# Kernel optimization log

Measured on AMD Instinct MI355X. Metric: run time of the kernel, lower is better.

Reference implementation:

```python
import jax, jax.numpy as jnp
import numpy as np
from jax import lax

B, C, H = 64, 3, 224
F = 8  # number of 3x3 filters
POOL = (H - 2) // 2  # 111
FEAT = POOL * POOL * F  # 98568


def setup_inputs() -> dict:
    key = jax.random.key(0)
    ks = jax.random.split(key, 8)
    return {
        "x": jax.random.normal(ks[0], (B, C, H, H), dtype=jnp.float32),
        "filters": jax.random.normal(ks[1], (F, 3, 3), dtype=jnp.float32),
        "W1": jax.random.normal(ks[2], (FEAT, 512), dtype=jnp.float32) * 0.01,
        "b1": jax.random.normal(ks[3], (512,), dtype=jnp.float32) * 0.01,
        "W2": jax.random.normal(ks[4], (512, 256), dtype=jnp.float32) * 0.02,
        "b2": jax.random.normal(ks[5], (256,), dtype=jnp.float32) * 0.02,
        "Wo": jax.random.normal(ks[6], (256, 1000), dtype=jnp.float32) * 0.02,
        "bo": jax.random.normal(ks[7], (1000,), dtype=jnp.float32) * 0.02,
    }


def reference(x, filters, W1, b1, W2, b2, Wo, bo):
    # conv_r + conv_g + conv_b == conv(r+g+b, filt) by linearity -> sum channels once
    s = x.sum(axis=1, keepdims=True)  # [B,1,H,H]
    k = filters[:, None, :, :]  # [F,1,3,3] (OIHW)
    conv = lax.conv_general_dilated(
        s, k, window_strides=(1, 1), padding="VALID",
        dimension_numbers=("NCHW", "OIHW", "NCHW"))  # [B,F,222,222]
    conv = jax.nn.relu(conv)
    pooled = lax.reduce_window(
        conv, -jnp.inf, lax.max,
        window_dimensions=(1, 1, 2, 2), window_strides=(1, 1, 2, 2),
        padding="VALID")  # [B,F,111,111]
    flat = pooled.reshape(x.shape[0], -1)  # filter-major layout matches torch cat order
    h = jax.nn.relu(flat @ W1 + b1)
    h = jax.nn.relu(h @ W2 + b2)
    return jax.nn.softmax(h @ Wo + bo, axis=1)
```

## Files before the change

### kernel.cpp

```cpp
#include <hip/hip_runtime.h>
#include <math.h>

#define Bsz 64
#define Himg 224
#define HS (Himg*Himg)
#define PW 111
#define PP (PW*PW)
#define Fn 8
#define FEAT (Fn*PP)
#define FEATP 98592
#define KC 32
#define NT32_TOT 3081
#define NCH 192
#define N1 512
#define N2 256
#define N3 1000
#define RG 8

typedef short short8 __attribute__((ext_vector_type(8)));
typedef float f32x4 __attribute__((ext_vector_type(4)));

#define GLOAD_LDS16(g, l)                                                     \
  __builtin_amdgcn_global_load_lds(                                           \
      (const __attribute__((address_space(1))) void*)(g),                     \
      (__attribute__((address_space(3))) void*)(l), 16, 0, 0)

__device__ __forceinline__ void cvt_hilo(const float* v, short8& hi, short8& lo) {
#pragma unroll
  for (int j = 0; j < 8; j++) {
    unsigned u = __builtin_bit_cast(unsigned, v[j]);
    hi[j] = (short)(u >> 16);
    float hf = __builtin_bit_cast(float, u & 0xFFFF0000u);
    float r = v[j] - hf;
    lo[j] = (short)(__builtin_bit_cast(unsigned, r) >> 16);
  }
}

__device__ __forceinline__ unsigned packhl(float f) {
  unsigned u = __builtin_bit_cast(unsigned, f);
  unsigned hi = u >> 16;
  float hf = __builtin_bit_cast(float, u & 0xFFFF0000u);
  float r = f - hf;
  unsigned lo = __builtin_bit_cast(unsigned, r) >> 16;
  return (hi << 16) | (lo & 0xFFFFu);
}

__device__ __forceinline__ uint4 pack4(float4 f) {
  uint4 o;
  o.x = packhl(f.x); o.y = packhl(f.y); o.z = packhl(f.z); o.w = packhl(f.w);
  return o;
}

__global__ void k_convpool(const float* __restrict__ x, const float* __restrict__ filt,
                           float* __restrict__ flat) {
  int i = blockIdx.x * 256 + threadIdx.x;
  if (i < Bsz * (FEATP - FEAT))
    flat[(size_t)(i / 24) * FEATP + FEAT + (i % 24)] = 0.f;
  if (i >= Bsz * PP) return;
  int b = i / PP, r = i - b * PP;
  int py = r / PW, px = r - py * PW;
  const float* xb = x + (size_t)b * 3 * HS + (size_t)(2 * py) * Himg + 2 * px;
  float p[4][4];
#pragma unroll
  for (int dy = 0; dy < 4; dy++) {
    const float* row = xb + dy * Himg;
    float2 a0 = *(const float2*)(row);
    float2 a1 = *(const float2*)(row + 2);
    float2 b0 = *(const float2*)(row + HS);
    float2 b1 = *(const float2*)(row + HS + 2);
    float2 c0 = *(const float2*)(row + 2 * HS);
    float2 c1 = *(const float2*)(row + 2 * HS + 2);
    p[dy][0] = a0.x + b0.x + c0.x;
    p[dy][1] = a0.y + b0.y + c0.y;
    p[dy][2] = a1.x + b1.x + c1.x;
    p[dy][3] = a1.y + b1.y + c1.y;
  }
  float* outb = flat + (size_t)b * FEATP + r;
#pragma unroll
  for (int f = 0; f < Fn; f++) {
    float mx = 0.f;
#pragma unroll
    for (int oy = 0; oy < 2; oy++)
#pragma unroll
      for (int ox = 0; ox < 2; ox++) {
        float c = 0.f;
#pragma unroll
        for (int dy = 0; dy < 3; dy++)
#pragma unroll
          for (int dx = 0; dx < 3; dx++)
            c = fmaf(p[oy + dy][ox + dx], filt[f * 9 + dy * 3 + dx], c);
        mx = fmaxf(mx, c);
      }
    outb[(size_t)f * PP] = mx;
  }
}

__global__ void __launch_bounds__(256) k_gemm1(const float* __restrict__ A,
                                               const float* __restrict__ W,
                                               float* __restrict__ partial) {
  __shared__ float Wl[2][KC][128];
  __shared__ unsigned As[2][64 * 32];
  const int t = threadIdx.x;
  const int wv = t >> 6;
  const int lane = t & 63;
  const int col0b = blockIdx.x * 128;
  const int c = blockIdx.y;
  const int tile0 = c * 16 + min(c, 9);
  const int nt = (c < 9) ? 17 : 16;
  const int lrow = lane & 15;
  const int lg8 = (lane >> 4) * 8;
  const int gr = lg8 >> 2;
  const int sr = wv * 16 + (lane >> 3);
  const int sq = lane & 7;
  const int sgs = ((sq ^ (sr & 7)) << 2);
  const float* Ast = A + (size_t)sr * FEATP + sq * 4;
  const int wsr = lane >> 5;
  const int wscx = ((lane & 31) * 4) ^ ((wv & 1) << 4);
  const int wcol = wv * 32 + lrow;
  const int wcolsw = wcol ^ (((lg8 >> 3) & 1) << 4);

  f32x4 acc[4][2];
#pragma unroll
  for (int mf = 0; mf < 4; mf++)
#pragma unroll
    for (int nf = 0; nf < 2; nf++)
#pragma unroll
      for (int r = 0; r < 4; r++) acc[mf][nf][r] = 0.f;

  float4 fa0, fa1;

#define STAGE_W(buf, kt)                                                      \
  {                                                                           \
    const int kb = (kt) * KC + wv * 8;                                        \
    _Pragma("unroll")                                                         \
    for (int p = 0; p < 4; p++) {                                             \
      int krow = kb + 2 * p + wsr;                                            \
      krow = krow < FEAT ? krow : FEAT - 1;       \
      GLOAD_LDS16(W + (size_t)krow * N1 + col0b + wscx,                       \
                  &Wl[buf][wv * 8 + 2 * p][0]);                               \
    }                                                                         \
  }

  auto loadA = [&](int kb) {
    fa0 = *(const float4*)(Ast + kb);
    fa1 = *(const float4*)(Ast + (size_t)8 * FEATP + kb);
  };
  auto writeA = [&](int buf) {
    *(uint4*)&As[buf][sr * 32 + sgs] = pack4(fa0);
    *(uint4*)&As[buf][(sr + 8) * 32 + sgs] = pack4(fa1);
  };

  STAGE_W(0, tile0)
  loadA(tile0 * KC);
  writeA(0);
  __syncthreads();

  for (int s = 0; s < nt; s++) {
    const int buf = s & 1;
    const bool more = (s + 1) < nt;
    if (more) {
      STAGE_W(buf ^ 1, tile0 + s + 1)
      loadA((tile0 + s + 1) * KC);
    }
    float bv0[8], bv1[8];
#pragma unroll
    for (int j = 0; j < 8; j++) {
      bv0[j] = Wl[buf][lg8 + j][wcolsw];
      bv1[j] = Wl[buf][lg8 + j][wcolsw ^ 16];
    }
    short8 bhi[2], blo[2];
    cvt_hilo(bv0, bhi[0], blo[0]);
    cvt_hilo(bv1, bhi[1], blo[1]);
#pragma unroll
    for (int mf = 0; mf < 4; mf++) {
      const int r = mf * 16 + lrow;
      const int key = (r & 7);
      unsigned au[8];
      *(uint4*)(au + 0) = *(const uint4*)&As[buf][r * 32 + ((gr ^ key) << 2)];
      *(uint4*)(au + 4) = *(const uint4*)&As[buf][r * 32 + (((gr + 1) ^ key) << 2)];
      short8 ahi, alo;
#pragma unroll
      for (int j = 0; j < 8; j++) {
        ahi[j] = (short)(au[j] >> 16);
        alo[j] = (short)(au[j] & 0xFFFFu);
      }
#pragma unroll
      for (int nf = 0; nf < 2; nf++) {
        acc[mf][nf] = __builtin_amdgcn_mfma_f32_16x16x32_bf16(ahi, bhi[nf], acc[mf][nf], 0, 0, 0);
        acc[mf][nf] = __builtin_amdgcn_mfma_f32_16x16x32_bf16(ahi, blo[nf], acc[mf][nf], 0, 0, 0);
        acc[mf][nf] = __builtin_amdgcn_mfma_f32_16x16x32_bf16(alo, bhi[nf], acc[mf][nf], 0, 0, 0);
      }
    }
    if (more) writeA(buf ^ 1);
    __syncthreads();
  }

  const int drow = (lane >> 4) * 4;
#pragma unroll
  for (int mf = 0; mf < 4; mf++) {
#pragma unroll
    for (int nf = 0; nf < 2; nf++) {
      float* pp = partial + ((size_t)c * Bsz + mf * 16 + drow) * N1 +
                  col0b + wv * 32 + nf * 16 + lrow;
#pragma unroll
      for (int r = 0; r < 4; r++) pp[(size_t)r * N1] = acc[mf][nf][r];
    }
  }
}

__global__ void k_red1a(const float* __restrict__ partial, float* __restrict__ partial2) {
  int i = blockIdx.x * 256 + threadIdx.x;
  int g = blockIdx.y;
  int c0 = g * 24;
  float sum = 0.f;
#pragma unroll 4
  for (int c = c0; c < c0 + 24; c++) sum += partial[(size_t)c * Bsz * N1 + i];
  partial2[(size_t)g * Bsz * N1 + i] = sum;
}

__global__ void __launch_bounds__(256) k_gemm2(const float* __restrict__ partial2,
                                               const float* __restrict__ b1,
                                               const float* __restrict__ W2,
                                               const float* __restrict__ b2,
                                               float* __restrict__ h2) {
  const int m = blockIdx.x >> 2;
  const int nq = blockIdx.x & 3;
  const int t = threadIdx.x;
  __shared__ float a[N1];
  __shared__ float red[4][64];
#pragma unroll
  for (int e = 0; e < 2; e++) {
    int idx = e * 256 + t;
    float sum = 0.f;
#pragma unroll
    for (int g = 0; g < RG; g++)
      sum += partial2[(size_t)g * Bsz * N1 + (size_t)m * N1 + idx];
    a[idx] = fmaxf(sum + b1[idx], 0.f);
  }
  __syncthreads();
  const int col = nq * 64 + (t & 63);
  const int ks = (t >> 6) * 128;
  float sum = 0.f;
#pragma unroll 8
  for (int k = 0; k < 128; k++)
    sum = fmaf(a[ks + k], W2[(size_t)(ks + k) * N2 + col], sum);
  red[t >> 6][t & 63] = sum;
  __syncthreads();
  if (t < 64) {
    float tot = red[0][t] + red[1][t] + red[2][t] + red[3][t] + b2[nq * 64 + t];
    h2[(size_t)m * N2 + nq * 64 + t] = fmaxf(tot, 0.f);
  }
}

__global__ void __launch_bounds__(256) k_logits(const float* __restrict__ h2,
                                                const float* __restrict__ Wo,
                                                const float* __restrict__ bo,
                                                float* __restrict__ logits) {
  const int m = blockIdx.x >> 2;
  const int nc = blockIdx.x & 3;
  const int t = threadIdx.x;
  __shared__ float a[N2];
  a[t] = h2[(size_t)m * N2 + t];
  __syncthreads();
  const int col = nc * 250 + t;
  if (t >= 250) return;
  float sum = bo[col];
#pragma unroll 8
  for (int k = 0; k < N2; k++)
    sum = fmaf(a[k], Wo[(size_t)k * N3 + col], sum);
  logits[(size_t)m * N3 + col] = sum;
}

__global__ void __launch_bounds__(256) k_softmax(const float* __restrict__ logits,
                                                 float* __restrict__ out) {
  const int m = blockIdx.x;
  const int t = threadIdx.x;
  __shared__ float red[8];
  float vals[4];
  float vmax = -3.4e38f;
#pragma unroll
  for (int j = 0; j < 4; j++) {
    int n = j * 256 + t;
    vals[j] = (n < N3) ? logits[(size_t)m * N3 + n] : -3.4e38f;
    vmax = fmaxf(vmax, vals[j]);
  }
#pragma unroll
  for (int off = 32; off > 0; off >>= 1) vmax = fmaxf(vmax, __shfl_xor(vmax, off));
  const int wid = t >> 6;
  if ((t & 63) == 0) red[wid] = vmax;
  __syncthreads();
  vmax = fmaxf(fmaxf(red[0], red[1]), fmaxf(red[2], red[3]));
  float ev[4];
  float esum = 0.f;
#pragma unroll
  for (int j = 0; j < 4; j++) {
    int n = j * 256 + t;
    float e = (n < N3) ? __expf(vals[j] - vmax) : 0.f;
    ev[j] = e;
    esum += e;
  }
#pragma unroll
  for (int off = 32; off > 0; off >>= 1) esum += __shfl_xor(esum, off);
  if ((t & 63) == 0) red[4 + wid] = esum;
  __syncthreads();
  esum = red[4] + red[5] + red[6] + red[7];
  float inv = 1.f / esum;
#pragma unroll
  for (int j = 0; j < 4; j++) {
    int n = j * 256 + t;
    if (n < N3) out[(size_t)m * N3 + n] = ev[j] * inv;
  }
}

extern "C" void kernel_launch(void* const* d_in, const int* in_sizes, int n_in,
                              void* d_out, int out_size, void* d_ws, size_t ws_size,
                              hipStream_t stream) {
  const float* x = (const float*)d_in[0];
  const float* filters = (const float*)d_in[1];
  const float* W1 = (const float*)d_in[2];
  const float* b1 = (const float*)d_in[3];
  const float* W2 = (const float*)d_in[4];
  const float* b2 = (const float*)d_in[5];
  const float* Wo = (const float*)d_in[6];
  const float* bo = (const float*)d_in[7];
  float* out = (float*)d_out;

  float* ws = (float*)d_ws;
  float* flat = ws;
  float* partial = flat + (size_t)Bsz * FEATP;
  float* partial2 = partial + (size_t)NCH * Bsz * N1;
  float* h2 = partial2 + (size_t)RG * Bsz * N1;
  float* logits = h2 + (size_t)Bsz * N2;

  k_convpool<<<(Bsz * PP + 255) / 256, 256, 0, stream>>>(x, filters, flat);
  dim3 g1(4, NCH);
  k_gemm1<<<g1, 256, 0, stream>>>(flat, W1, partial);
  dim3 gr(Bsz * N1 / 256, RG);
  k_red1a<<<gr, 256, 0, stream>>>(partial, partial2);
  k_gemm2<<<Bsz * 4, 256, 0, stream>>>(partial2, b1, W2, b2, h2);
  k_logits<<<Bsz * 4, 256, 0, stream>>>(h2, Wo, bo, logits);
  k_softmax<<<Bsz, 256, 0, stream>>>(logits, out);
}
```

Before: 99.25 us.

## Pre-split activations to bf16 hi/lo in convpool and DMA them into LDS

The conv+pool kernel now writes each pooled activation already packed as a bf16 hi/lo pair, so the split is no longer repeated in the GEMM. The GEMM's A tile is then staged with direct global-to-LDS loads, using an XOR-swizzled source address, instead of register loads followed by a pack and an LDS store. This removes packing ALU work and register traffic from the GEMM's main loop and lets the A loads overlap with compute asynchronously, the same way the W loads already do. The risk is that the swizzled global gather pattern makes the direct-to-LDS loads less coalesced.

```diff
diff --git a/kernel.cpp b/kernel.cpp
--- a/kernel.cpp
+++ b/kernel.cpp
@@ -45,17 +45,11 @@
   return (hi << 16) | (lo & 0xFFFFu);
 }
 
-__device__ __forceinline__ uint4 pack4(float4 f) {
-  uint4 o;
-  o.x = packhl(f.x); o.y = packhl(f.y); o.z = packhl(f.z); o.w = packhl(f.w);
-  return o;
-}
-
 __global__ void k_convpool(const float* __restrict__ x, const float* __restrict__ filt,
-                           float* __restrict__ flat) {
+                           unsigned* __restrict__ flat) {
   int i = blockIdx.x * 256 + threadIdx.x;
   if (i < Bsz * (FEATP - FEAT))
-    flat[(size_t)(i / 24) * FEATP + FEAT + (i % 24)] = 0.f;
+    flat[(size_t)(i / 24) * FEATP + FEAT + (i % 24)] = 0u;
   if (i >= Bsz * PP) return;
   int b = i / PP, r = i - b * PP;
   int py = r / PW, px = r - py * PW;
@@ -75,7 +69,7 @@
     p[dy][2] = a1.x + b1.x + c1.x;
     p[dy][3] = a1.y + b1.y + c1.y;
   }
-  float* outb = flat + (size_t)b * FEATP + r;
+  unsigned* outb = flat + (size_t)b * FEATP + r;
 #pragma unroll
   for (int f = 0; f < Fn; f++) {
     float mx = 0.f;
@@ -91,11 +85,11 @@
             c = fmaf(p[oy + dy][ox + dx], filt[f * 9 + dy * 3 + dx], c);
         mx = fmaxf(mx, c);
       }
-    outb[(size_t)f * PP] = mx;
-  }
-}
-
-__global__ void __launch_bounds__(256) k_gemm1(const float* __restrict__ A,
+    outb[(size_t)f * PP] = packhl(mx);
+  }
+}
+
+__global__ void __launch_bounds__(256) k_gemm1(const unsigned* __restrict__ Ap,
                                                const float* __restrict__ W,
                                                float* __restrict__ partial) {
   __shared__ float Wl[2][KC][128];
@@ -110,14 +104,12 @@
   const int lrow = lane & 15;
   const int lg8 = (lane >> 4) * 8;
   const int gr = lg8 >> 2;
-  const int sr = wv * 16 + (lane >> 3);
-  const int sq = lane & 7;
-  const int sgs = ((sq ^ (sr & 7)) << 2);
-  const float* Ast = A + (size_t)sr * FEATP + sq * 4;
   const int wsr = lane >> 5;
   const int wscx = ((lane & 31) * 4) ^ ((wv & 1) << 4);
   const int wcol = wv * 32 + lrow;
   const int wcolsw = wcol ^ (((lg8 >> 3) & 1) << 4);
+  const int asr = lane >> 3;
+  const int ags = (lane & 7) ^ asr;
 
   f32x4 acc[4][2];
 #pragma unroll
@@ -126,8 +118,6 @@
     for (int nf = 0; nf < 2; nf++)
 #pragma unroll
       for (int r = 0; r < 4; r++) acc[mf][nf][r] = 0.f;
-
-  float4 fa0, fa1;
 
 #define STAGE_W(buf, kt)                                                      \
   {                                                                           \
@@ -140,19 +130,18 @@
                   &Wl[buf][wv * 8 + 2 * p][0]);                               \
     }                                                                         \
   }
-
-  auto loadA = [&](int kb) {
-    fa0 = *(const float4*)(Ast + kb);
-    fa1 = *(const float4*)(Ast + (size_t)8 * FEATP + kb);
-  };
-  auto writeA = [&](int buf) {
-    *(uint4*)&As[buf][sr * 32 + sgs] = pack4(fa0);
-    *(uint4*)&As[buf][(sr + 8) * 32 + sgs] = pack4(fa1);
-  };
+#define STAGE_A(buf, kt)                                                      \
+  {                                                                           \
+    const int kb = (kt) * KC;                                                 \
+    _Pragma("unroll")                                                         \
+    for (int e = 0; e < 2; e++) {                                             \
+      GLOAD_LDS16(Ap + (size_t)(wv * 16 + e * 8 + asr) * FEATP + kb + ags * 4,\
+                  &As[buf][(wv * 16 + e * 8) * 32]);                          \
+    }                                                                         \
+  }
 
   STAGE_W(0, tile0)
-  loadA(tile0 * KC);
-  writeA(0);
+  STAGE_A(0, tile0)
   __syncthreads();
 
   for (int s = 0; s < nt; s++) {
@@ -160,7 +149,7 @@
     const bool more = (s + 1) < nt;
     if (more) {
       STAGE_W(buf ^ 1, tile0 + s + 1)
-      loadA((tile0 + s + 1) * KC);
+      STAGE_A(buf ^ 1, tile0 + s + 1)
     }
     float bv0[8], bv1[8];
 #pragma unroll
@@ -191,7 +180,6 @@
         acc[mf][nf] = __builtin_amdgcn_mfma_f32_16x16x32_bf16(alo, bhi[nf], acc[mf][nf], 0, 0, 0);
       }
     }
-    if (more) writeA(buf ^ 1);
     __syncthreads();
   }
 
@@ -326,8 +314,8 @@
   float* out = (float*)d_out;
 
   float* ws = (float*)d_ws;
-  float* flat = ws;
-  float* partial = flat + (size_t)Bsz * FEATP;
+  unsigned* flat = (unsigned*)ws;
+  float* partial = ws + (size_t)Bsz * FEATP;
   float* partial2 = partial + (size_t)NCH * Bsz * N1;
   float* h2 = partial2 + (size_t)RG * Bsz * N1;
   float* logits = h2 + (size_t)Bsz * N2;
```

Result: slower. 102.8 us (+3.6%).
